# Performance work log

Hardware: AMD Instinct MI355X
Metric: run time of the kernel (lower is better)

The kernel has to match this reference:

```python
import jax, jax.numpy as jnp
import numpy as np

HIDDEN = 4096
N_HEADS = 16
HEAD_DIM = HIDDEN // N_HEADS  # 256
ROTARY_DIM = 64
ROPE_THETA = 10000.0


def _rope_cos_sin(positions):
    # positions: [S] int -> cos/sin: [S, ROTARY_DIM//2]
    inv_freq = 1.0 / (ROPE_THETA ** (jnp.arange(0, ROTARY_DIM, 2, dtype=jnp.float32) / ROTARY_DIM))
    angles = positions.astype(jnp.float32)[:, None] * inv_freq[None, :]
    return jnp.cos(angles), jnp.sin(angles)


def _apply_rope_interleaved(x, cos, sin):
    # x: [B, S, H, D]; rotate first ROTARY_DIM dims, GPT-J (non-neox) interleaved pairs
    xr = x[..., :ROTARY_DIM]
    x1 = xr[..., 0::2]
    x2 = xr[..., 1::2]
    c = cos[None, :, None, :]
    s = sin[None, :, None, :]
    o1 = x1 * c - x2 * s
    o2 = x1 * s + x2 * c
    rot = jnp.stack([o1, o2], axis=-1).reshape(xr.shape)
    return jnp.concatenate([rot, x[..., ROTARY_DIM:]], axis=-1)


def setup_inputs() -> dict:
    key = jax.random.key(0)
    k1, k2, k3 = jax.random.split(key, 3)
    B, S = 2, 2048
    hidden_states = jax.random.normal(k1, (B, S, HIDDEN), dtype=jnp.float32)
    positions = jnp.arange(S, dtype=jnp.int32)
    w_qkv = jax.random.normal(k2, (3 * HIDDEN, HIDDEN), dtype=jnp.float32) * 0.02
    w_out = jax.random.normal(k3, (HIDDEN, HIDDEN), dtype=jnp.float32) * 0.02
    return {"hidden_states": hidden_states, "positions": positions, "w_qkv": w_qkv, "w_out": w_out}


def reference(hidden_states, positions, w_qkv, w_out):
    B, S, H = hidden_states.shape
    qkv = jnp.einsum("bsh,oh->bso", hidden_states, w_qkv)  # [B,S,3H]
    q, k, v = jnp.split(qkv, 3, axis=-1)
    q = q.reshape(B, S, N_HEADS, HEAD_DIM)
    k = k.reshape(B, S, N_HEADS, HEAD_DIM)
    v = v.reshape(B, S, N_HEADS, HEAD_DIM)
    cos, sin = _rope_cos_sin(positions)
    q = _apply_rope_interleaved(q, cos, sin)
    k = _apply_rope_interleaved(k, cos, sin)
    scale = HEAD_DIM ** -0.5
    scores = jnp.einsum("bqhd,bkhd->bhqk", q, k) * scale  # [B,nh,S,S]
    causal = jnp.tril(jnp.ones((S, S), dtype=bool))
    scores = jnp.where(causal[None, None], scores, jnp.finfo(scores.dtype).min)
    probs = jax.nn.softmax(scores, axis=-1)
    attn = jnp.einsum("bhqk,bkhd->bqhd", probs, v).reshape(B, S, H)
    return jnp.einsum("bsh,oh->bso", attn, w_out)
```

## Files before the change

### kernel.cpp

```cpp
#include <hip/hip_runtime.h>

typedef __attribute__((ext_vector_type(8))) short short8;
typedef __attribute__((ext_vector_type(4))) float f32x4;

__device__ __forceinline__ unsigned short f2bf(float f) {
    union { float f; unsigned int u; } v; v.f = f;
    unsigned int u = v.u;
    unsigned int r = (u + 0x7FFFu + ((u >> 16) & 1u)) >> 16;
    return (unsigned short)r;
}
__device__ __forceinline__ float bf2f(unsigned short u) {
    union { unsigned int u; float f; } v; v.u = ((unsigned int)u) << 16;
    return v.f;
}
__device__ __forceinline__ void load_lds16(const void* g, void* l) {
    __builtin_amdgcn_global_load_lds(
        (const __attribute__((address_space(1))) void*)g,
        (__attribute__((address_space(3))) void*)l, 16, 0, 0);
}
#define BAR() asm volatile("s_barrier" ::: "memory")
#define WAITV(n) asm volatile("s_waitcnt vmcnt(" #n ")" ::: "memory")

__device__ __forceinline__ int swz(int o) { return o ^ ((o >> 3) & 0x70); }

__global__ __launch_bounds__(256) void conv_bf16(const float* __restrict__ in,
                                                 unsigned short* __restrict__ out, int n4) {
    int i = blockIdx.x * 256 + threadIdx.x;
    if (i >= n4) return;
    float4 v = ((const float4*)in)[i];
    ushort4 o;
    o.x = f2bf(v.x); o.y = f2bf(v.y); o.z = f2bf(v.z); o.w = f2bf(v.w);
    ((ushort4*)out)[i] = o;
}

template <bool OUT_BF16>
__global__ __launch_bounds__(512, 2) void gemm256(const unsigned short* __restrict__ A,
                                                  const unsigned short* __restrict__ B,
                                                  void* __restrict__ Cv,
                                                  int M, int N, int K, int NBN) {
    __shared__ __align__(16) char smem[131072];
    const int tid = threadIdx.x;
    const int lane = tid & 63, wv = tid >> 6;
    const int wm = wv >> 2, wn = wv & 3;
    const int fr = lane & 15, fo = (lane >> 4) * 8;

    const int nwg = gridDim.x, bid = blockIdx.x;
    const int q = nwg >> 3, r = nwg & 7, xcd = bid & 7, lid = bid >> 3;
    const int wg = (xcd < r ? xcd * (q + 1) : r * (q + 1) + (xcd - r) * q) + lid;
    const int bm = wg / NBN, bn = wg % NBN;

    const unsigned short* gA = A + (size_t)bm * 256 * K;
    const unsigned short* gB = B + (size_t)bn * 256 * K;

    int srow[2][2], scol[2][2];
#pragma unroll
    for (int h = 0; h < 2; ++h)
#pragma unroll
        for (int rr = 0; rr < 2; ++rr) {
            int o = h * 16384 + rr * 8192 + tid * 16;
            int osw = swz(o);
            srow[h][rr] = osw >> 7;
            scol[h][rr] = (osw & 127) >> 1;
        }

    f32x4 acc[8][4] = {};
    short8 a[4][2], b[4][2];

    auto STAGE = [&](const unsigned short* g, int regionBase, int h, int t) {
#pragma unroll
        for (int rr = 0; rr < 2; ++rr)
            load_lds16(g + (size_t)srow[h][rr] * K + t * 64 + scol[h][rr],
                       smem + regionBase + h * 16384 + rr * 8192 + tid * 16);
    };
    auto RDA = [&](int bufBase, int mh) {
#pragma unroll
        for (int mf = 0; mf < 4; ++mf)
#pragma unroll
            for (int ks = 0; ks < 2; ++ks) {
                int o = swz((wm * 128 + mh * 64 + mf * 16 + fr) * 128 + (ks * 32 + fo) * 2);
                a[mf][ks] = *(const short8*)(smem + bufBase + o);
            }
    };
    auto RDB = [&](int bufBase, int nh) {
#pragma unroll
        for (int jj = 0; jj < 2; ++jj)
#pragma unroll
            for (int ks = 0; ks < 2; ++ks) {
                int o = swz((wn * 64 + (nh * 2 + jj) * 16 + fr) * 128 + (ks * 32 + fo) * 2);
                b[nh * 2 + jj][ks] = *(const short8*)(smem + bufBase + 32768 + o);
            }
    };
    auto MM = [&](int mh, int nh) {
        __builtin_amdgcn_s_setprio(1);
#pragma unroll
        for (int mf = 0; mf < 4; ++mf)
#pragma unroll
            for (int jj = 0; jj < 2; ++jj)
#pragma unroll
                for (int ks = 0; ks < 2; ++ks)
                    acc[mh * 4 + mf][nh * 2 + jj] = __builtin_amdgcn_mfma_f32_16x16x32_bf16(
                        a[mf][ks], b[nh * 2 + jj][ks], acc[mh * 4 + mf][nh * 2 + jj], 0, 0, 0);
        __builtin_amdgcn_s_setprio(0);
    };

    const int A0 = 0, B0 = 32768, A1 = 65536, B1 = 98304;

    STAGE(gA, A0, 0, 0); STAGE(gA, A0, 1, 0);
    STAGE(gB, B0, 0, 0); STAGE(gB, B0, 1, 0);
    STAGE(gB, B1, 0, 1); STAGE(gB, B1, 1, 1);
    STAGE(gA, A1, 0, 1); STAGE(gA, A1, 1, 1);
    WAITV(8);
    BAR();
    RDA(A0, 0);
    RDB(A0, 0);

    const int NIT = K >> 7;
    for (int i = 0; i < NIT; ++i) {
        const bool last = (i == NIT - 1);
        const int t2 = 2 * i + 2, t3 = 2 * i + 3;
        RDB(A0, 1);
        MM(0, 0);
        if (i > 0) STAGE(gA, A1, 1, 2 * i + 1);
        BAR();
        MM(0, 1);
        RDA(A0, 1);
        BAR();
        MM(1, 1);
        if (!last) {
            STAGE(gB, B0, 0, t2);
            WAITV(2);
        } else {
            WAITV(0);
        }
        BAR();
        MM(1, 0);
        RDA(A1, 0); RDB(A1, 0);
        if (!last) { STAGE(gB, B0, 1, t2); STAGE(gA, A0, 0, t2); }
        BAR();
        RDB(A1, 1);
        MM(0, 0);
        if (!last) STAGE(gA, A0, 1, t2);
        BAR();
        MM(0, 1);
        RDA(A1, 1);
        BAR();
        MM(1, 1);
        if (!last) {
            STAGE(gB, B1, 0, t3);
            WAITV(2);
        }
        BAR();
        MM(1, 0);
        if (!last) {
            RDA(A0, 0); RDB(A0, 0);
            STAGE(gB, B1, 1, t3); STAGE(gA, A1, 0, t3);
        }
        BAR();
    }

    const size_t row0 = (size_t)bm * 256 + wm * 128 + ((lane >> 4) << 2);
    const int col0 = bn * 256 + wn * 64 + fr;
#pragma unroll
    for (int mf = 0; mf < 8; ++mf)
#pragma unroll
        for (int nf = 0; nf < 4; ++nf)
#pragma unroll
            for (int j = 0; j < 4; ++j) {
                size_t idx = (row0 + mf * 16 + j) * (size_t)N + col0 + nf * 16;
                if (OUT_BF16) ((unsigned short*)Cv)[idx] = f2bf(acc[mf][nf][j]);
                else          ((float*)Cv)[idx] = acc[mf][nf][j];
            }
}

__global__ __launch_bounds__(256) void rope_repack(const unsigned short* __restrict__ qkv,
                                                   const int* __restrict__ positions,
                                                   unsigned short* __restrict__ qp,
                                                   unsigned short* __restrict__ kp) {
    int r = blockIdx.x * 4 + (threadIdx.x >> 6);
    int h = r & 15, s = (r >> 4) & 2047, b = r >> 15;
    int d = (threadIdx.x & 63) * 4;
    const unsigned short* src = qkv + (size_t)(b * 2048 + s) * 12288 + h * 256 + d;
    ushort4 q = *(const ushort4*)src;
    ushort4 k = *(const ushort4*)(src + 4096);
    if (d < 64) {
        float pos = (float)positions[s];
        const float LF = 0.4152410118609203f;
        float i0 = (float)(d >> 1);
        float a0 = pos * exp2f(-i0 * LF);
        float a1 = pos * exp2f(-(i0 + 1.0f) * LF);
        float c0 = cosf(a0), s0 = sinf(a0), c1 = cosf(a1), s1 = sinf(a1);
        float qx = bf2f(q.x), qy = bf2f(q.y), qz = bf2f(q.z), qw = bf2f(q.w);
        q.x = f2bf(qx * c0 - qy * s0); q.y = f2bf(qx * s0 + qy * c0);
        q.z = f2bf(qz * c1 - qw * s1); q.w = f2bf(qz * s1 + qw * c1);
        float kx = bf2f(k.x), ky = bf2f(k.y), kz = bf2f(k.z), kw = bf2f(k.w);
        k.x = f2bf(kx * c0 - ky * s0); k.y = f2bf(kx * s0 + ky * c0);
        k.z = f2bf(kz * c1 - kw * s1); k.w = f2bf(kz * s1 + kw * c1);
    }
    size_t dst = ((size_t)((b * 16 + h) * 2048 + s)) * 256 + d;
    *(ushort4*)&qp[dst] = q;
    *(ushort4*)&kp[dst] = k;
}

__global__ __launch_bounds__(256) void v_transpose(const unsigned short* __restrict__ qkv,
                                                   unsigned short* __restrict__ vt) {
    int bid = blockIdx.x;
    int dt = bid & 3, st = (bid >> 2) & 31, bh = bid >> 7;
    int b = bh >> 4, h = bh & 15;
    __shared__ unsigned short t[64][72];
    int tid = threadIdx.x;
#pragma unroll
    for (int rep = 0; rep < 16; ++rep) {
        int idx = rep * 256 + tid;
        int r = idx >> 6, c = idx & 63;
        t[r][c] = qkv[(size_t)(b * 2048 + st * 64 + r) * 12288 + 8192 + h * 256 + dt * 64 + c];
    }
    __syncthreads();
#pragma unroll
    for (int rep = 0; rep < 16; ++rep) {
        int idx = rep * 256 + tid;
        int r = idx >> 6, c = idx & 63;
        vt[(size_t)(bh * 256 + dt * 64 + r) * 2048 + st * 64 + c] = t[c][r];
    }
}

__global__ __launch_bounds__(256) void attn_fwd(const unsigned short* __restrict__ Qp,
                                                const unsigned short* __restrict__ Kp,
                                                const unsigned short* __restrict__ Vt,
                                                unsigned short* __restrict__ Oa) {
    __shared__ __align__(16) unsigned short Ks[32 * 256];
    __shared__ __align__(16) unsigned short Vs[256 * 32];
    __shared__ __align__(16) char Ps[4 * 16 * 80];
    const int tid = threadIdx.x, lane = tid & 63, wv = tid >> 6;
    const int bh = blockIdx.x, qt = blockIdx.y;
    const int fr = lane & 15, g = lane >> 4, fo = g * 8;
    const unsigned short* Qb = Qp + (size_t)bh * 2048 * 256;
    const unsigned short* Kb = Kp + (size_t)bh * 2048 * 256;
    const unsigned short* Vb = Vt + (size_t)bh * 256 * 2048;
    const int qbase = qt * 64 + wv * 16;
    char* PsW = Ps + wv * 1280;

    short8 qf[8];
#pragma unroll
    for (int c = 0; c < 8; ++c)
        qf[c] = *(const short8*)&Qb[(size_t)(qbase + fr) * 256 + c * 32 + fo];

    f32x4 o_acc[16] = {};
    float m_run = -1e30f, l_run = 0.f;
    const int qi = qbase + fr;

    const int nkv = qt * 64 + 64;
    for (int kv0 = 0; kv0 < nkv; kv0 += 32) {
#pragma unroll
        for (int i = 0; i < 4; ++i) {
            int ob = (wv * 4 + i) * 1024 + lane * 16;
            int osw = ob ^ ((ob >> 5) & 0x70);
            int row = kv0 + (ob >> 9);
            load_lds16(&Kb[(size_t)row * 256 + ((osw & 511) >> 1)],
                       (char*)Ks + (wv * 4 + i) * 1024);
        }
#pragma unroll
        for (int i = 0; i < 4; ++i) {
            int ob = (wv * 4 + i) * 1024 + lane * 16;
            int osw = ob ^ ((((ob >> 6) ^ (ob >> 8)) & 3) << 4);
            int drow = ob >> 6;
            load_lds16(&Vb[(size_t)drow * 2048 + kv0 + ((osw & 63) >> 1)],
                       (char*)Vs + (wv * 4 + i) * 1024);
        }
        __syncthreads();

        f32x4 sc[2] = {};
#pragma unroll
        for (int tt = 0; tt < 2; ++tt)
#pragma unroll
            for (int c = 0; c < 8; ++c) {
                int o = (tt * 16 + fr) * 512 + (c * 32 + fo) * 2;
                o ^= (o >> 5) & 0x70;
                short8 kf = *(const short8*)((const char*)Ks + o);
                sc[tt] = __builtin_amdgcn_mfma_f32_16x16x32_bf16(kf, qf[c], sc[tt], 0, 0, 0);
            }

        float sv[2][4];
        float pmax = -1e30f;
#pragma unroll
        for (int tt = 0; tt < 2; ++tt)
#pragma unroll
            for (int j = 0; j < 4; ++j) {
                int kvi = kv0 + tt * 16 + g * 4 + j;
                float x = sc[tt][j] * 0.0625f;
                sv[tt][j] = (kvi > qi) ? -1e30f : x;
                pmax = fmaxf(pmax, sv[tt][j]);
            }
        pmax = fmaxf(pmax, __shfl_xor(pmax, 16));
        pmax = fmaxf(pmax, __shfl_xor(pmax, 32));

        if (__any(pmax > m_run + 8.f)) {
            float mn = fmaxf(m_run, pmax);
            float al = __expf(m_run - mn);
            m_run = mn;
            l_run *= al;
            float alj[4];
#pragma unroll
            for (int j = 0; j < 4; ++j) alj[j] = __shfl(al, g * 4 + j);
#pragma unroll
            for (int n = 0; n < 16; ++n) {
                o_acc[n][0] *= alj[0]; o_acc[n][1] *= alj[1];
                o_acc[n][2] *= alj[2]; o_acc[n][3] *= alj[3];
            }
        }

        float rs = 0.f;
#pragma unroll
        for (int tt = 0; tt < 2; ++tt) {
            float p0 = __expf(sv[tt][0] - m_run);
            float p1 = __expf(sv[tt][1] - m_run);
            float p2 = __expf(sv[tt][2] - m_run);
            float p3 = __expf(sv[tt][3] - m_run);
            rs += (p0 + p1) + (p2 + p3);
            ushort4 pk;
            pk.x = f2bf(p0); pk.y = f2bf(p1); pk.z = f2bf(p2); pk.w = f2bf(p3);
            *(ushort4*)(PsW + fr * 80 + tt * 32 + g * 8) = pk;
        }
        rs += __shfl_xor(rs, 16);
        rs += __shfl_xor(rs, 32);
        l_run += rs;

        short8 pf = *(const short8*)(PsW + fr * 80 + g * 16);
#pragma unroll
        for (int n = 0; n < 16; ++n) {
            int o = (n * 16 + fr) * 64 + fo * 2;
            o ^= (((o >> 6) ^ (o >> 8)) & 3) << 4;
            short8 vf = *(const short8*)((const char*)Vs + o);
            o_acc[n] = __builtin_amdgcn_mfma_f32_16x16x32_bf16(pf, vf, o_acc[n], 0, 0, 0);
        }
        __syncthreads();
    }

    const int b = bh >> 4, h = bh & 15;
    float linv = 1.0f / l_run;
#pragma unroll
    for (int j = 0; j < 4; ++j) {
        float inv = __shfl(linv, g * 4 + j);
        int qrow = qbase + g * 4 + j;
        size_t base = ((size_t)(b * 2048 + qrow)) * 4096 + h * 256;
#pragma unroll
        for (int n = 0; n < 16; ++n)
            Oa[base + n * 16 + fr] = f2bf(o_acc[n][j] * inv);
    }
}

extern "C" void kernel_launch(void* const* d_in, const int* in_sizes, int n_in,
                              void* d_out, int out_size, void* d_ws, size_t ws_size,
                              hipStream_t stream) {
    const float* hidden = (const float*)d_in[0];
    const int* positions = (const int*)d_in[1];
    const float* w_qkv = (const float*)d_in[2];
    const float* w_out = (const float*)d_in[3];
    float* out = (float*)d_out;

    const size_t MB32 = 33554432;
    char* ws = (char*)d_ws;
    unsigned short* hidden_bf = (unsigned short*)ws;
    unsigned short* wqkv_bf   = (unsigned short*)(ws + MB32);
    unsigned short* qkv_bf    = (unsigned short*)(ws + 4 * MB32);
    unsigned short* qp  = wqkv_bf;
    unsigned short* kp  = wqkv_bf + 16777216;
    unsigned short* vtp = wqkv_bf + 33554432;
    unsigned short* attn_bf = hidden_bf;
    unsigned short* wout_bf = qkv_bf;

    conv_bf16<<<16384, 256, 0, stream>>>(hidden, hidden_bf, 4194304);
    conv_bf16<<<49152, 256, 0, stream>>>(w_qkv, wqkv_bf, 12582912);

    gemm256<true><<<16 * 48, 512, 0, stream>>>(hidden_bf, wqkv_bf, qkv_bf, 4096, 12288, 4096, 48);

    rope_repack<<<16384, 256, 0, stream>>>(qkv_bf, positions, qp, kp);
    v_transpose<<<4096, 256, 0, stream>>>(qkv_bf, vtp);

    attn_fwd<<<dim3(32, 32), 256, 0, stream>>>(qp, kp, vtp, attn_bf);

    conv_bf16<<<16384, 256, 0, stream>>>(w_out, wout_bf, 4194304);
    gemm256<false><<<16 * 16, 512, 0, stream>>>(attn_bf, wout_bf, out, 4096, 4096, 4096, 16);
}
```

Before: 729.1 us.

## Prefetch next K/V tile into registers to overlap loads with compute

```diff
diff --git a/kernel.cpp b/kernel.cpp
--- a/kernel.cpp
+++ b/kernel.cpp
@@ -239,6 +239,19 @@
     const int qbase = qt * 64 + wv * 16;
     char* PsW = Ps + wv * 1280;
 
+    const unsigned short* ksrc[4];
+    const unsigned short* vsrc[4];
+    int dstb[4];
+#pragma unroll
+    for (int i = 0; i < 4; ++i) {
+        int ob = (wv * 4 + i) * 1024 + lane * 16;
+        dstb[i] = ob;
+        int oswK = ob ^ ((ob >> 5) & 0x70);
+        ksrc[i] = Kb + (size_t)(ob >> 9) * 256 + ((oswK & 511) >> 1);
+        int oswV = ob ^ ((((ob >> 6) ^ (ob >> 8)) & 3) << 4);
+        vsrc[i] = Vb + (size_t)(ob >> 6) * 2048 + ((oswV & 63) >> 1);
+    }
+
     short8 qf[8];
 #pragma unroll
     for (int c = 0; c < 8; ++c)
@@ -248,25 +261,28 @@
     float m_run = -1e30f, l_run = 0.f;
     const int qi = qbase + fr;
 
+    float4 kpre[4], vpre[4];
+#pragma unroll
+    for (int i = 0; i < 4; ++i) kpre[i] = *(const float4*)(ksrc[i]);
+#pragma unroll
+    for (int i = 0; i < 4; ++i) vpre[i] = *(const float4*)(vsrc[i]);
+
     const int nkv = qt * 64 + 64;
     for (int kv0 = 0; kv0 < nkv; kv0 += 32) {
 #pragma unroll
-        for (int i = 0; i < 4; ++i) {
-            int ob = (wv * 4 + i) * 1024 + lane * 16;
-            int osw = ob ^ ((ob >> 5) & 0x70);
-            int row = kv0 + (ob >> 9);
-            load_lds16(&Kb[(size_t)row * 256 + ((osw & 511) >> 1)],
-                       (char*)Ks + (wv * 4 + i) * 1024);
-        }
-#pragma unroll
-        for (int i = 0; i < 4; ++i) {
-            int ob = (wv * 4 + i) * 1024 + lane * 16;
-            int osw = ob ^ ((((ob >> 6) ^ (ob >> 8)) & 3) << 4);
-            int drow = ob >> 6;
-            load_lds16(&Vb[(size_t)drow * 2048 + kv0 + ((osw & 63) >> 1)],
-                       (char*)Vs + (wv * 4 + i) * 1024);
-        }
+        for (int i = 0; i < 4; ++i) *(float4*)((char*)Ks + dstb[i]) = kpre[i];
+#pragma unroll
+        for (int i = 0; i < 4; ++i) *(float4*)((char*)Vs + dstb[i]) = vpre[i];
         __syncthreads();
+
+        if (kv0 + 32 < nkv) {
+#pragma unroll
+            for (int i = 0; i < 4; ++i)
+                kpre[i] = *(const float4*)(ksrc[i] + (size_t)(kv0 + 32) * 256);
+#pragma unroll
+            for (int i = 0; i < 4; ++i)
+                vpre[i] = *(const float4*)(vsrc[i] + (kv0 + 32));
+        }
 
         f32x4 sc[2] = {};
 #pragma unroll
```

Result: slower. 1.081 ms (+48.3%).
